# Performance work log

Measured on AMD Instinct MI355X. Metric: run time of the kernel, lower is better.

## Reference

```python
import jax
jax.config.update('jax_enable_x64', True)
import jax.numpy as jnp
import numpy as np

B = 262144
MASK = 0xFFFFFFFF

K_CONST = [1116352408, 1899447441, 3049323471, 3921009573, 961987163, 1508970993, 2453635748, 2870763221, 3624381080, 310598401, 607225278, 1426881987, 1925078388, 2162078206, 2614888103, 3248222580, 3835390401, 4022224774, 264347078, 604807628, 770255983, 1249150122, 1555081692, 1996064986, 2554220882, 2821834349, 2952996808, 3210313671, 3336571891, 3584528711, 113926993, 338241895, 666307205, 773529912, 1294757372, 1396182291, 1695183700, 1986661051, 2177026350, 2456956037, 2730485921, 2820302411, 3259730800, 3345764771, 3516065817, 3600352804, 4094571909, 275423344, 430227734, 506948616, 659060556, 883997877, 958139571, 1322822218, 1537002063, 1747873779, 1955562222, 2024104815, 2227730452, 2361852424, 2428436474, 2756734187, 3204031479, 3329325298]
H0_CONST = [1779033703, 3144134277, 1013904242, 2773480762, 1359893119, 2600822924, 528734635, 1541459225]


def setup_inputs() -> dict:
    key = jax.random.key(0)
    messages = jax.random.randint(key, (B, 64), 0, 256, dtype=jnp.int64)
    return {"messages": messages}


def _rotr(x, n):
    # x holds a 32-bit value in an int64; emulate 32-bit rotate-right
    return ((x >> n) | (x << (32 - n))) & MASK


def reference(messages) -> jnp.ndarray:
    m = messages.astype(jnp.int64)
    # pack 4 bytes -> 16 big-endian 32-bit words, vectorized over batch: (B,16)
    words = (m[:, 0::4] << 24) | (m[:, 1::4] << 16) | (m[:, 2::4] << 8) | m[:, 3::4]

    # message schedule expansion to 64 words (fixed 48-iteration unroll, batched)
    W = [words[:, i] for i in range(16)]
    for i in range(16, 64):
        x15, x2 = W[i - 15], W[i - 2]
        s0 = (_rotr(x15, 7) ^ _rotr(x15, 18) ^ (x15 >> 3)) & MASK
        s1 = (_rotr(x2, 17) ^ _rotr(x2, 19) ^ (x2 >> 10)) & MASK
        W.append((W[i - 16] + s0 + W[i - 7] + s1) & MASK)

    # compression: 64 rounds, fully batched (each var is (B,))
    ones = jnp.ones((messages.shape[0],), dtype=jnp.int64)
    a, b_, c, d, e, f, g, h = [ones * hv for hv in H0_CONST]
    for i in range(64):
        S1 = (_rotr(e, 6) ^ _rotr(e, 11) ^ _rotr(e, 25)) & MASK
        ch = ((e & f) ^ (~e & g)) & MASK
        temp1 = (h + S1 + ch + K_CONST[i] + W[i]) & MASK
        S0 = (_rotr(a, 2) ^ _rotr(a, 13) ^ _rotr(a, 22)) & MASK
        maj = ((a & b_) ^ (a & c) ^ (b_ & c)) & MASK
        temp2 = (S0 + maj) & MASK
        h, g, f = g, f, e
        e = (d + temp1) & MASK
        d, c, b_ = c, b_, a
        a = (temp1 + temp2) & MASK

    out = jnp.stack([
        (H0_CONST[0] + a) & MASK, (H0_CONST[1] + b_) & MASK,
        (H0_CONST[2] + c) & MASK, (H0_CONST[3] + d) & MASK,
        (H0_CONST[4] + e) & MASK, (H0_CONST[5] + f) & MASK,
        (H0_CONST[6] + g) & MASK, (H0_CONST[7] + h) & MASK,
    ], axis=1)  # (B, 8)
    return out
```

## Files before the change

kernel.cpp:

```cpp
#include <hip/hip_runtime.h>
#include <stdint.h>

constexpr uint32_t Kc[64] = {
    1116352408u, 1899447441u, 3049323471u, 3921009573u,  961987163u, 1508970993u,
    2453635748u, 2870763221u, 3624381080u,  310598401u,  607225278u, 1426881987u,
    1925078388u, 2162078206u, 2614888103u, 3248222580u, 3835390401u, 4022224774u,
     264347078u,  604807628u,  770255983u, 1249150122u, 1555081692u, 1996064986u,
    2554220882u, 2821834349u, 2952996808u, 3210313671u, 3336571891u, 3584528711u,
     113926993u,  338241895u,  666307205u,  773529912u, 1294757372u, 1396182291u,
    1695183700u, 1986661051u, 2177026350u, 2456956037u, 2730485921u, 2820302411u,
    3259730800u, 3345764771u, 3516065817u, 3600352804u, 4094571909u,  275423344u,
     430227734u,  506948616u,  659060556u,  883997877u,  958139571u, 1322822218u,
    1537002063u, 1747873779u, 1955562222u, 2024104815u, 2227730452u, 2361852424u,
    2428436474u, 2756734187u, 3204031479u, 3329325298u
};

#define ROTR(x,n) (((x) >> (n)) | ((x) << (32 - (n))))

#define RND(a,b,c,d,e,f,g,h,K,w) {                                        \
    uint32_t t1 = h + (ROTR(e,6) ^ ROTR(e,11) ^ ROTR(e,25))               \
                    + ((e & f) ^ (~e & g)) + (K) + (w);                   \
    uint32_t nx = a ^ b;                                                  \
    uint32_t t2 = (ROTR(a,2) ^ ROTR(a,13) ^ ROTR(a,22)) + (b ^ (nx & xab)); \
    xab = nx;                                                             \
    d += t1; h = t1 + t2; }

#define R0(K,w) RND(a,b,c,d,e,f,g,h,K,w)
#define R1(K,w) RND(h,a,b,c,d,e,f,g,K,w)
#define R2(K,w) RND(g,h,a,b,c,d,e,f,K,w)
#define R3(K,w) RND(f,g,h,a,b,c,d,e,K,w)
#define R4(K,w) RND(e,f,g,h,a,b,c,d,K,w)
#define R5(K,w) RND(d,e,f,g,h,a,b,c,K,w)
#define R6(K,w) RND(c,d,e,f,g,h,a,b,K,w)
#define R7(K,w) RND(b,c,d,e,f,g,h,a,K,w)

#define WEXP(wA,wB,wC,wD)                                                 \
    wA += (ROTR(wB,7) ^ ROTR(wB,18) ^ ((wB) >> 3)) + (wC)                 \
        + (ROTR(wD,17) ^ ROTR(wD,19) ^ ((wD) >> 10));

__device__ __forceinline__ uint32_t pack_be(int4 v) {
    return ((uint32_t)v.x << 24) | ((uint32_t)v.y << 16) |
           ((uint32_t)v.z << 8)  |  (uint32_t)v.w;
}

__global__ __launch_bounds__(256) void sha256_kernel(
        const int* __restrict__ msg, uint32_t* __restrict__ out, int n) {
    const uint32_t tid = blockIdx.x * blockDim.x + threadIdx.x;
    if (tid >= (uint32_t)n) return;

    const int4* m4 = reinterpret_cast<const int4*>(msg) + (size_t)tid * 16;

    uint32_t w0  = pack_be(m4[0]),  w1  = pack_be(m4[1]);
    uint32_t w2  = pack_be(m4[2]),  w3  = pack_be(m4[3]);
    uint32_t w4  = pack_be(m4[4]),  w5  = pack_be(m4[5]);
    uint32_t w6  = pack_be(m4[6]),  w7  = pack_be(m4[7]);
    uint32_t w8  = pack_be(m4[8]),  w9  = pack_be(m4[9]);
    uint32_t w10 = pack_be(m4[10]), w11 = pack_be(m4[11]);
    uint32_t w12 = pack_be(m4[12]), w13 = pack_be(m4[13]);
    uint32_t w14 = pack_be(m4[14]), w15 = pack_be(m4[15]);

    uint32_t a = 1779033703u, b = 3144134277u, c = 1013904242u, d = 2773480762u;
    uint32_t e = 1359893119u, f = 2600822924u, g =  528734635u, h = 1541459225u;
    uint32_t xab = b ^ c;

    R0(Kc[0],w0)  R1(Kc[1],w1)  R2(Kc[2],w2)  R3(Kc[3],w3)
    R4(Kc[4],w4)  R5(Kc[5],w5)  R6(Kc[6],w6)  R7(Kc[7],w7)
    R0(Kc[8],w8)  R1(Kc[9],w9)  R2(Kc[10],w10) R3(Kc[11],w11)
    R4(Kc[12],w12) R5(Kc[13],w13) R6(Kc[14],w14) R7(Kc[15],w15)

    WEXP(w0,w1,w9,w14)    R0(Kc[16],w0)
    WEXP(w1,w2,w10,w15)   R1(Kc[17],w1)
    WEXP(w2,w3,w11,w0)    R2(Kc[18],w2)
    WEXP(w3,w4,w12,w1)    R3(Kc[19],w3)
    WEXP(w4,w5,w13,w2)    R4(Kc[20],w4)
    WEXP(w5,w6,w14,w3)    R5(Kc[21],w5)
    WEXP(w6,w7,w15,w4)    R6(Kc[22],w6)
    WEXP(w7,w8,w0,w5)     R7(Kc[23],w7)
    WEXP(w8,w9,w1,w6)     R0(Kc[24],w8)
    WEXP(w9,w10,w2,w7)    R1(Kc[25],w9)
    WEXP(w10,w11,w3,w8)   R2(Kc[26],w10)
    WEXP(w11,w12,w4,w9)   R3(Kc[27],w11)
    WEXP(w12,w13,w5,w10)  R4(Kc[28],w12)
    WEXP(w13,w14,w6,w11)  R5(Kc[29],w13)
    WEXP(w14,w15,w7,w12)  R6(Kc[30],w14)
    WEXP(w15,w0,w8,w13)   R7(Kc[31],w15)

    WEXP(w0,w1,w9,w14)    R0(Kc[32],w0)
    WEXP(w1,w2,w10,w15)   R1(Kc[33],w1)
    WEXP(w2,w3,w11,w0)    R2(Kc[34],w2)
    WEXP(w3,w4,w12,w1)    R3(Kc[35],w3)
    WEXP(w4,w5,w13,w2)    R4(Kc[36],w4)
    WEXP(w5,w6,w14,w3)    R5(Kc[37],w5)
    WEXP(w6,w7,w15,w4)    R6(Kc[38],w6)
    WEXP(w7,w8,w0,w5)     R7(Kc[39],w7)
    WEXP(w8,w9,w1,w6)     R0(Kc[40],w8)
    WEXP(w9,w10,w2,w7)    R1(Kc[41],w9)
    WEXP(w10,w11,w3,w8)   R2(Kc[42],w10)
    WEXP(w11,w12,w4,w9)   R3(Kc[43],w11)
    WEXP(w12,w13,w5,w10)  R4(Kc[44],w12)
    WEXP(w13,w14,w6,w11)  R5(Kc[45],w13)
    WEXP(w14,w15,w7,w12)  R6(Kc[46],w14)
    WEXP(w15,w0,w8,w13)   R7(Kc[47],w15)

    WEXP(w0,w1,w9,w14)    R0(Kc[48],w0)
    WEXP(w1,w2,w10,w15)   R1(Kc[49],w1)
    WEXP(w2,w3,w11,w0)    R2(Kc[50],w2)
    WEXP(w3,w4,w12,w1)    R3(Kc[51],w3)
    WEXP(w4,w5,w13,w2)    R4(Kc[52],w4)
    WEXP(w5,w6,w14,w3)    R5(Kc[53],w5)
    WEXP(w6,w7,w15,w4)    R6(Kc[54],w6)
    WEXP(w7,w8,w0,w5)     R7(Kc[55],w7)
    WEXP(w8,w9,w1,w6)     R0(Kc[56],w8)
    WEXP(w9,w10,w2,w7)    R1(Kc[57],w9)
    WEXP(w10,w11,w3,w8)   R2(Kc[58],w10)
    WEXP(w11,w12,w4,w9)   R3(Kc[59],w11)
    WEXP(w12,w13,w5,w10)  R4(Kc[60],w12)
    WEXP(w13,w14,w6,w11)  R5(Kc[61],w13)
    WEXP(w14,w15,w7,w12)  R6(Kc[62],w14)
    WEXP(w15,w0,w8,w13)   R7(Kc[63],w15)

    uint4* o = reinterpret_cast<uint4*>(out) + (size_t)tid * 2;
    o[0] = make_uint4(1779033703u + a, 3144134277u + b,
                      1013904242u + c, 2773480762u + d);
    o[1] = make_uint4(1359893119u + e, 2600822924u + f,
                       528734635u + g, 1541459225u + h);
}

extern "C" void kernel_launch(void* const* d_in, const int* in_sizes, int n_in,
                              void* d_out, int out_size, void* d_ws, size_t ws_size,
                              hipStream_t stream) {
    const int* msg = (const int*)d_in[0];
    uint32_t* out = (uint32_t*)d_out;
    const int n = in_sizes[0] / 64;
    const int block = 256;
    const int grid = (n + block - 1) / block;
    sha256_kernel<<<grid, block, 0, stream>>>(msg, out, n);
}
```

Measured before the change: 99.38 us.

## Stage message loads through swizzled LDS for coalesced global reads

In the old code each thread read its own 256-byte message with strided int4 loads, so a wavefront's accesses were uncoalesced. The block now loads its messages cooperatively with consecutive int4 reads, writes them to shared memory using an XOR swizzle to avoid bank conflicts, synchronises, and each thread then reads its own 16 words from LDS. The block size drops to 128, which keeps LDS at 32 KB per block. The cost is an extra barrier and LDS traffic. The bounds check now applies only to the store, so a partial final block would read past the input.

```diff
diff --git a/kernel.cpp b/kernel.cpp
--- a/kernel.cpp
+++ b/kernel.cpp
@@ -43,21 +43,33 @@
            ((uint32_t)v.z << 8)  |  (uint32_t)v.w;
 }
 
-__global__ __launch_bounds__(256) void sha256_kernel(
+#define BLOCK 128
+
+__global__ __launch_bounds__(BLOCK) void sha256_kernel(
         const int* __restrict__ msg, uint32_t* __restrict__ out, int n) {
-    const uint32_t tid = blockIdx.x * blockDim.x + threadIdx.x;
-    if (tid >= (uint32_t)n) return;
+    const int t = threadIdx.x;
+    const uint32_t m = blockIdx.x * BLOCK + t;
 
-    const int4* m4 = reinterpret_cast<const int4*>(msg) + (size_t)tid * 16;
+    __shared__ int4 lds[BLOCK * 16];
 
-    uint32_t w0  = pack_be(m4[0]),  w1  = pack_be(m4[1]);
-    uint32_t w2  = pack_be(m4[2]),  w3  = pack_be(m4[3]);
-    uint32_t w4  = pack_be(m4[4]),  w5  = pack_be(m4[5]);
-    uint32_t w6  = pack_be(m4[6]),  w7  = pack_be(m4[7]);
-    uint32_t w8  = pack_be(m4[8]),  w9  = pack_be(m4[9]);
-    uint32_t w10 = pack_be(m4[10]), w11 = pack_be(m4[11]);
-    uint32_t w12 = pack_be(m4[12]), w13 = pack_be(m4[13]);
-    uint32_t w14 = pack_be(m4[14]), w15 = pack_be(m4[15]);
+    const int4* gbase = reinterpret_cast<const int4*>(msg)
+                      + (size_t)blockIdx.x * BLOCK * 16;
+#pragma unroll
+    for (int it = 0; it < 16; ++it) {
+        int g = it * BLOCK + t;
+        int4 v = gbase[g];
+        int owner = g >> 4;
+        int j = g & 15;
+        lds[owner * 16 + (j ^ (owner & 15))] = v;
+    }
+    __syncthreads();
+
+#define LOADW(j) pack_be(lds[t * 16 + ((j) ^ (t & 15))])
+    uint32_t w0  = LOADW(0),  w1  = LOADW(1),  w2  = LOADW(2),  w3  = LOADW(3);
+    uint32_t w4  = LOADW(4),  w5  = LOADW(5),  w6  = LOADW(6),  w7  = LOADW(7);
+    uint32_t w8  = LOADW(8),  w9  = LOADW(9),  w10 = LOADW(10), w11 = LOADW(11);
+    uint32_t w12 = LOADW(12), w13 = LOADW(13), w14 = LOADW(14), w15 = LOADW(15);
+#undef LOADW
 
     uint32_t a = 1779033703u, b = 3144134277u, c = 1013904242u, d = 2773480762u;
     uint32_t e = 1359893119u, f = 2600822924u, g =  528734635u, h = 1541459225u;
@@ -119,11 +131,13 @@
     WEXP(w14,w15,w7,w12)  R6(Kc[62],w14)
     WEXP(w15,w0,w8,w13)   R7(Kc[63],w15)
 
-    uint4* o = reinterpret_cast<uint4*>(out) + (size_t)tid * 2;
-    o[0] = make_uint4(1779033703u + a, 3144134277u + b,
-                      1013904242u + c, 2773480762u + d);
-    o[1] = make_uint4(1359893119u + e, 2600822924u + f,
-                       528734635u + g, 1541459225u + h);
+    if (m < (uint32_t)n) {
+        uint4* o = reinterpret_cast<uint4*>(out) + (size_t)m * 2;
+        o[0] = make_uint4(1779033703u + a, 3144134277u + b,
+                          1013904242u + c, 2773480762u + d);
+        o[1] = make_uint4(1359893119u + e, 2600822924u + f,
+                           528734635u + g, 1541459225u + h);
+    }
 }
 
 extern "C" void kernel_launch(void* const* d_in, const int* in_sizes, int n_in,
@@ -132,7 +146,6 @@
     const int* msg = (const int*)d_in[0];
     uint32_t* out = (uint32_t*)d_out;
     const int n = in_sizes[0] / 64;
-    const int block = 256;
-    const int grid = (n + block - 1) / block;
-    sha256_kernel<<<grid, block, 0, stream>>>(msg, out, n);
+    const int grid = (n + BLOCK - 1) / BLOCK;
+    sha256_kernel<<<grid, BLOCK, 0, stream>>>(msg, out, n);
 }
```

Result: no change. 100.9 us (+1.5%).
